# Performance work log

Measured on AMD Instinct MI355X. Metric: run time of the kernel, lower is better.

Reference implementation:

```python
import jax, jax.numpy as jnp
import numpy as np

U = 256    # hp.hidden_size * 2 (attention num_units / encoder dim)
H = 128    # hp.hidden_size (prenet output, attn GRU input)
MEL = 80   # hp.decoder_output_dim == hp.num_mels
R = 5      # hp.outputs_per_step
B = 64
T = 1000


def _glorot(key, shape):
    fan_in = shape[-1]
    return jax.random.normal(key, shape, jnp.float32) / jnp.sqrt(jnp.float32(fan_in))


def setup_inputs() -> dict:
    key = jax.random.key(0)
    ks = jax.random.split(key, 16)
    p = {}
    p["memory"] = jax.random.normal(ks[0], (B, T, U), jnp.float32)
    # prenet: fc1 (MEL->U), fc2 (U->H)
    p["Wp1"] = _glorot(ks[1], (U, MEL)); p["bp1"] = jnp.zeros((U,), jnp.float32)
    p["Wp2"] = _glorot(ks[2], (H, U));   p["bp2"] = jnp.zeros((H,), jnp.float32)
    # Bahdanau attention params (no bias)
    p["W1"] = _glorot(ks[3], (U, U))
    p["W2"] = _glorot(ks[4], (U, U))
    p["v"]  = _glorot(ks[5], (U,))
    def gru(k, din):
        k1, k2 = jax.random.split(k)
        return (_glorot(k1, (3 * U, din)), _glorot(k2, (3 * U, U)),
                jnp.zeros((3 * U,), jnp.float32), jnp.zeros((3 * U,), jnp.float32))
    p["Wa_ih"], p["Wa_hh"], p["ba_ih"], p["ba_hh"] = gru(ks[6], H)
    p["W1_ih"], p["W1_hh"], p["b1_ih"], p["b1_hh"] = gru(ks[7], U)
    p["W2_ih"], p["W2_hh"], p["b2_ih"], p["b2_hh"] = gru(ks[8], U)
    p["Wproj"] = _glorot(ks[9], (U, 2 * U)); p["bproj"] = jnp.zeros((U,), jnp.float32)
    p["Wout"] = _glorot(ks[10], (MEL * R, U)); p["bout"] = jnp.zeros((MEL * R,), jnp.float32)
    return p


def _gru_cell(x, h, W_ih, W_hh, b_ih, b_hh):
    # torch.nn.GRUCell semantics
    gi = x @ W_ih.T + b_ih
    gh = h @ W_hh.T + b_hh
    ir, iz, inn = jnp.split(gi, 3, axis=-1)
    hr, hz, hn = jnp.split(gh, 3, axis=-1)
    r = jax.nn.sigmoid(ir + hr)
    z = jax.nn.sigmoid(iz + hz)
    n = jnp.tanh(inn + r * hn)
    return (1.0 - z) * n + z * h


def reference(memory, Wp1, bp1, Wp2, bp2, W1, W2, v,
              Wa_ih, Wa_hh, ba_ih, ba_hh,
              W1_ih, W1_hh, b1_ih, b1_hh,
              W2_ih, W2_hh, b2_ih, b2_hh,
              Wproj, bproj, Wout, bout):
    b, t, u = memory.shape
    steps = t // R  # training branch: timesteps = memory_len // outputs_per_step
    # keys = W1(memory): constant across timesteps, hoist out of the loop
    keys = jnp.einsum('btu,vu->btv', memory, W1)
    init = (jnp.zeros((b, MEL), memory.dtype),  # prev mel frame (GO frame = zeros)
            jnp.zeros((b, u), memory.dtype),    # attn_hidden
            jnp.zeros((b, u), memory.dtype),    # gru1_hidden
            jnp.zeros((b, u), memory.dtype))    # gru2_hidden

    def step(carry, _):
        prev, attn_h, g1_h, g2_h = carry
        # prenet (dropout omitted for determinism; identity in eval mode)
        x = jax.nn.relu(prev @ Wp1.T + bp1)
        x = jax.nn.relu(x @ Wp2.T + bp2)
        # attention query through GRU cell
        d_t = _gru_cell(x, attn_h, Wa_ih, Wa_hh, ba_ih, ba_hh)
        q = d_t @ W2.T                                     # [b,u]
        scores = jnp.tanh(keys + q[:, None, :]) @ v       # [b,t]
        aw = jax.nn.softmax(scores, axis=1)
        d_t_prime = jnp.einsum('bt,btu->bu', aw, memory)   # context
        # residual GRU stack
        g1_in = jnp.concatenate([d_t, d_t_prime], axis=1) @ Wproj.T + bproj
        g1_h = _gru_cell(g1_in, g1_h, W1_ih, W1_hh, b1_ih, b1_hh)
        g2_in = g1_in + g1_h
        g2_h = _gru_cell(g2_in, g2_h, W2_ih, W2_hh, b2_ih, b2_hh)
        out = ((g2_in + g2_h) @ Wout.T + bout).reshape(b, MEL, R)
        return (out[:, :, -1], d_t, g1_h, g2_h), out

    _, ys = jax.lax.scan(step, init, None, length=steps)   # [steps,b,MEL,R]
    # torch.cat(outputs, 2) -> [b, MEL, steps*R]
    return jnp.transpose(ys, (1, 2, 0, 3)).reshape(b, MEL, steps * R)
```

## Files before the change

kernel.cpp:

```cpp
#include <hip/hip_runtime.h>

typedef _Float16 f16;
typedef _Float16 h2 __attribute__((ext_vector_type(2)));
typedef float fv4 __attribute__((ext_vector_type(4)));

#define BB 64
#define UU 256
#define RRR 5
#define NQUAD 4

constexpr size_t O_WP1T = 0;
constexpr size_t O_WP2T = 10240;
constexpr size_t O_WAIH = 26624;
constexpr size_t O_WAHH = 75776;
constexpr size_t O_WQP  = 174080;
constexpr size_t O_WPC  = 239616;
constexpr size_t O_W1IH = 272384;
constexpr size_t O_W1HH = 370688;
constexpr size_t O_W2IH = 468992;
constexpr size_t O_W2HH = 567296;
constexpr size_t O_WOUT = 665600;
constexpr size_t OF_BQP = 716800;
constexpr size_t OF_W1T = 717312;
constexpr size_t OH_KEYS = 1565696;
constexpr size_t OH_MEM  = OH_KEYS + 16384000;
constexpr size_t OF_CTXP  = 17166848;
constexpr size_t OF_ESUM  = 17297920;
constexpr size_t OI_FLAGS = 17298432;

#define SCL2LOG2E 2.8853900817779268f

#if defined(__has_builtin)
#if __has_builtin(__builtin_amdgcn_fdot2)
#define USE_FDOT2 1
#endif
#endif

__device__ __forceinline__ float dot2f(h2 a, h2 b, float c){
#ifdef USE_FDOT2
  return __builtin_amdgcn_fdot2(a, b, c, false);
#else
  return c + (float)a[0]*(float)b[0] + (float)a[1]*(float)b[1];
#endif
}

__device__ __forceinline__ float frcp(float x){ return __builtin_amdgcn_rcpf(x); }
__device__ __forceinline__ float fexp2(float x){ return __builtin_amdgcn_exp2f(x); }
__device__ __forceinline__ float fsig(float x){ return frcp(1.0f + fexp2(-1.4426950408889634f*x)); }
__device__ __forceinline__ float ftanh(float x){ return 1.0f - 2.0f*frcp(1.0f + fexp2(SCL2LOG2E*x)); }

__global__ void k_tr_hx(const float* __restrict__ src, int srcK, int kbase,
                        h2* __restrict__ dst, int N, int K, int Ntot, int coloff,
                        float scale){
  int idx = blockIdx.x*blockDim.x + threadIdx.x;
  int tot = N*(K/2);
  if (idx < tot){
    int k2 = idx / N, n = idx - k2*N;
    h2 p; p[0]=(f16)(scale*src[n*srcK + kbase + 2*k2]);
    p[1]=(f16)(scale*src[n*srcK + kbase + 2*k2+1]);
    dst[(size_t)k2*Ntot + coloff + n] = p;
  }
}

__global__ void k_transpose(const float* __restrict__ src, float* __restrict__ dst, int N, int K){
  int idx = blockIdx.x*blockDim.x + threadIdx.x;
  if (idx < N*K){
    int n = idx / K, k = idx - n*K;
    dst[k*N + n] = src[idx];
  }
}

__global__ void k_biasqp(const float* __restrict__ bproj, float* __restrict__ dst){
  int i = blockIdx.x*blockDim.x + threadIdx.x;
  if (i < 512) dst[i] = (i < 256) ? 0.f : bproj[i-256];
}

__global__ void k_zero(int* __restrict__ p, int n){
  int i = blockIdx.x*blockDim.x + threadIdx.x;
  if (i < n) p[i] = 0;
}

__global__ void k_memh(const float* __restrict__ src, f16* __restrict__ dst, int n8){
  int i = blockIdx.x*blockDim.x + threadIdx.x;
  if (i < n8){
    const float4* s = reinterpret_cast<const float4*>(src) + 2*(size_t)i;
    float4 f0 = s[0], f1 = s[1];
    union { f16 h[8]; float4 v; } u;
    u.h[0]=(f16)f0.x; u.h[1]=(f16)f0.y; u.h[2]=(f16)f0.z; u.h[3]=(f16)f0.w;
    u.h[4]=(f16)f1.x; u.h[5]=(f16)f1.y; u.h[6]=(f16)f1.z; u.h[7]=(f16)f1.w;
    reinterpret_cast<float4*>(dst)[i] = u.v;
  }
}

__global__ __launch_bounds__(256) void k_keys(const float* __restrict__ mem,
      const float* __restrict__ W1t, f16* __restrict__ keys, int T)
{
  const int b = blockIdx.z;
  const int tbase = blockIdx.x * 128;
  const int cbase = blockIdx.y * 128;
  const int tid = threadIdx.x;
  const int rt = tid >> 4, ct = tid & 15;
  const float* memb = mem + (size_t)b*T*UU;

  float acc[8][8];
  #pragma unroll
  for (int i=0;i<8;i++){
    #pragma unroll
    for (int j=0;j<8;j++) acc[i][j]=0.f;
  }
  const float* arow[8];
  #pragma unroll
  for (int i=0;i<8;i++){
    int t = tbase + rt*8 + i;
    arow[i] = memb + (size_t)(t < T ? t : T-1)*UU;
  }
  const float* wcol = W1t + cbase + ct*8;

  for (int k=0;k<UU;k+=4){
    float w8[4][8];
    #pragma unroll
    for (int kk=0;kk<4;kk++){
      float4 lo = *reinterpret_cast<const float4*>(wcol + (size_t)(k+kk)*UU);
      float4 hi = *reinterpret_cast<const float4*>(wcol + (size_t)(k+kk)*UU + 4);
      w8[kk][0]=lo.x; w8[kk][1]=lo.y; w8[kk][2]=lo.z; w8[kk][3]=lo.w;
      w8[kk][4]=hi.x; w8[kk][5]=hi.y; w8[kk][6]=hi.z; w8[kk][7]=hi.w;
    }
    #pragma unroll
    for (int i=0;i<8;i++){
      float4 a = *reinterpret_cast<const float4*>(arow[i] + k);
      float a4[4] = {a.x, a.y, a.z, a.w};
      #pragma unroll
      for (int kk=0;kk<4;kk++){
        #pragma unroll
        for (int j=0;j<8;j++) acc[i][j] += a4[kk]*w8[kk][j];
      }
    }
  }
  #pragma unroll
  for (int i=0;i<8;i++){
    int t = tbase + rt*8 + i;
    if (t < T){
      f16* dst = keys + (size_t)b*T*UU + (size_t)t*UU + cbase + ct*8;
      union { f16 h[8]; float4 v; } u;
      #pragma unroll
      for (int j=0;j<8;j++) u.h[j] = (f16)(acc[i][j]*SCL2LOG2E);
      *reinterpret_cast<float4*>(dst) = u.v;
    }
  }
}

__device__ __attribute__((noinline)) void gemv_shfl(
    const h2* __restrict__ W, const h2* __restrict__ in,
    const float* __restrict__ bias, float* __restrict__ destf, h2* __restrict__ desth,
    int K2, int Nf4, int act, int local)
{
  const int lane = local & 63;
  const int half = lane >> 5;
  int col = (local >> 6)*32 + (lane & 31);
  const bool valid = col < Nf4;
  if (!valid) col = 0;
  const int kh = K2 >> 1;
  const float4* w = reinterpret_cast<const float4*>(W) + (size_t)(half*kh)*Nf4 + col;
  const h2* ia = in + half*kh;
  float a0=0.f, a1=0.f, a2=0.f, a3=0.f;
  #pragma unroll 8
  for (int it = 0; it < kh; ++it){
    float4 wp = w[(size_t)it*Nf4];
    h2 a = ia[it];
    const h2* wh = reinterpret_cast<const h2*>(&wp);
    a0 = dot2f(wh[0], a, a0);
    a1 = dot2f(wh[1], a, a1);
    a2 = dot2f(wh[2], a, a2);
    a3 = dot2f(wh[3], a, a3);
  }
  a0 += __shfl_xor(a0, 32, 64);
  a1 += __shfl_xor(a1, 32, 64);
  a2 += __shfl_xor(a2, 32, 64);
  a3 += __shfl_xor(a3, 32, 64);
  if (half == 0 && valid){
    if (bias){
      const float4 bv = reinterpret_cast<const float4*>(bias)[col];
      a0+=bv.x; a1+=bv.y; a2+=bv.z; a3+=bv.w;
    }
    if (act == 1){
      a0=fmaxf(a0,0.f); a1=fmaxf(a1,0.f); a2=fmaxf(a2,0.f); a3=fmaxf(a3,0.f);
    } else if (act == 2){
      const float4 d = reinterpret_cast<float4*>(destf)[col];
      a0+=d.x; a1+=d.y; a2+=d.z; a3+=d.w;
    }
    if (destf){
      float4 r; r.x=a0; r.y=a1; r.z=a2; r.w=a3;
      reinterpret_cast<float4*>(destf)[col] = r;
    }
    if (desth){
      h2 p0; p0[0]=(f16)a0; p0[1]=(f16)a1;
      h2 p1; p1[0]=(f16)a2; p1[1]=(f16)a3;
      desth[2*col] = p0; desth[2*col+1] = p1;
    }
  }
}

__device__ __attribute__((noinline)) void gru_gate(
    const float* __restrict__ gi, const float* __restrict__ gh,
    float* __restrict__ h, h2* __restrict__ hh2,
    const float* __restrict__ addsrc, float* __restrict__ sumf,
    h2* __restrict__ sumh, int tid)
{
  if (tid < 128){
    float hn[2], sm[2] = {0.f, 0.f};
    #pragma unroll
    for (int d=0; d<2; ++d){
      int e = 2*tid + d;
      float r = fsig(gi[e] + gh[e]);
      float z = fsig(gi[256+e] + gh[256+e]);
      float n = ftanh(gi[512+e] + r*gh[512+e]);
      hn[d] = (1.f - z)*n + z*h[e];
      h[e] = hn[d];
      if (addsrc){ sm[d] = addsrc[e] + hn[d]; if (sumf) sumf[e] = sm[d]; }
    }
    h2 p; p[0]=(f16)hn[0]; p[1]=(f16)hn[1];
    hh2[tid] = p;
    if (addsrc && sumh){ h2 q; q[0]=(f16)sm[0]; q[1]=(f16)sm[1]; sumh[tid] = q; }
  }
  __syncthreads();
}

__global__ __launch_bounds__(1024) void k_decode(
    const h2* __restrict__ wts, const float* __restrict__ wsf,
    const f16* __restrict__ keysg, const f16* __restrict__ memg,
    float* __restrict__ ctxp, float* __restrict__ esum, int* __restrict__ flags,
    const float* __restrict__ bp1, const float* __restrict__ bp2,
    const float* __restrict__ vvec,
    const float* __restrict__ ba_ih, const float* __restrict__ ba_hh,
    const float* __restrict__ b1_ih, const float* __restrict__ b1_hh,
    const float* __restrict__ b2_ih, const float* __restrict__ b2_hh,
    const float* __restrict__ bout,
    float* __restrict__ out, int T, int steps)
{
  __shared__ __align__(16) float s_red[4096];
  __shared__ __align__(16) float s_sc[1024];
  __shared__ __align__(16) float s_gi[768];
  __shared__ __align__(16) float s_gh[768];
  __shared__ __align__(16) float s_gh1[768];
  __shared__ __align__(16) float s_gh2[768];
  __shared__ __align__(16) float s_q[512];
  __shared__ __align__(16) float s_ha[256];
  __shared__ __align__(16) float s_g1h[256];
  __shared__ __align__(16) float s_g2h[256];
  __shared__ __align__(16) float s_g2in[256];
  __shared__ __align__(16) float s_y[400];
  __shared__ __align__(16) f16   s_prevf[80];
  __shared__ __align__(16) h2    s_hah[128], s_g1hh[128], s_g2hh[128];
  __shared__ __align__(16) h2    s_g1inh[128], s_g2inh[128], s_s2h[128];
  __shared__ __align__(16) h2    s_x1h[128], s_xh[64], s_ctxh[128];
  __shared__ float s_wred[16];

  const int b    = blockIdx.x & 63;
  const int quad = blockIdx.x >> 6;
  const int tid = threadIdx.x;
  const int lane = tid & 63;
  const int wid = tid >> 6;
  const int half_id = lane >> 5;
  const int cl = lane & 31;

  const f16* keyb = keysg + (size_t)b*T*UU;
  const f16* memb = memg  + (size_t)b*T*UU;
  float* outb = out + (size_t)b*80*(steps*RRR);
  const int tq0 = (T*quad)/NQUAD, tq1 = (T*(quad+1))/NQUAD;

  if (tid < 128){
    s_ha[2*tid]=0.f; s_ha[2*tid+1]=0.f;
    s_g1h[2*tid]=0.f; s_g1h[2*tid+1]=0.f;
    s_g2h[2*tid]=0.f; s_g2h[2*tid+1]=0.f;
    h2 z; z[0]=(f16)0.f; z[1]=(f16)0.f;
    s_hah[tid]=z; s_g1hh[tid]=z; s_g2hh[tid]=z;
  }
  if (tid < 80) s_prevf[tid] = (f16)0.f;
  __syncthreads();

  float v8[8], m8[8];
  #pragma unroll
  for (int j=0;j<8;j++){ v8[j] = vvec[cl*8+j]; m8[j] = -2.0f*v8[j]; }
  float sumv = 0.f;
  #pragma unroll
  for (int j=0;j<8;j++) sumv += v8[j];
  #pragma unroll
  for (int o=1;o<32;o<<=1) sumv += __shfl_xor(sumv, o);

  for (int step = 0; step < steps; ++step){
    const int par = step & 1;
    if (tid < 384)      gemv_shfl(wts+O_WAHH, s_hah,  ba_hh, s_gh,  nullptr, 128, 192, 0, tid);
    else if (tid < 768) gemv_shfl(wts+O_W1HH, s_g1hh, b1_hh, s_gh1, nullptr, 128, 192, 0, tid-384);
    else if (tid < 896) gemv_shfl(wts+O_WP1T, reinterpret_cast<const h2*>(s_prevf), bp1,
                                  nullptr, s_x1h, 40, 64, 1, tid-768);
    __syncthreads();
    if (tid < 384)      gemv_shfl(wts+O_W2HH, s_g2hh, b2_hh, s_gh2, nullptr, 128, 192, 0, tid);
    else if (tid < 448) gemv_shfl(wts+O_WP2T, s_x1h, bp2, nullptr, s_xh, 128, 32, 1, tid-384);
    __syncthreads();
    if (tid < 384) gemv_shfl(wts+O_WAIH, s_xh, ba_ih, s_gi, nullptr, 64, 192, 0, tid);
    __syncthreads();
    gru_gate(s_gi, s_gh, s_ha, s_hah, nullptr, nullptr, nullptr, tid);
    if (tid < 256) gemv_shfl(wts+O_WQP, s_hah, wsf+OF_BQP, s_q, nullptr, 128, 128, 0, tid);
    __syncthreads();

    {
      float q8[8];
      #pragma unroll
      for (int j=0;j<8;j++) q8[j] = s_q[cl*8+j];
      float rs = 0.f;
      for (int t0 = tq0 + wid*2; t0 < tq1; t0 += 32){
        int t = t0 + half_id;
        fv4 kv = *(reinterpret_cast<const fv4*>(keyb + (size_t)t*UU) + cl);
        const h2* kh = reinterpret_cast<const h2*>(&kv);
        float acc = 0.f;
        #pragma unroll
        for (int p=0;p<4;p++){
          float t0f = (float)kh[p][0] + q8[2*p];
          float t1f = (float)kh[p][1] + q8[2*p+1];
          acc = fmaf(m8[2*p],   frcp(1.f + fexp2(t0f)), acc);
          acc = fmaf(m8[2*p+1], frcp(1.f + fexp2(t1f)), acc);
        }
        #pragma unroll
        for (int o=1;o<32;o<<=1) acc += __shfl_xor(acc, o);
        float e = __expf(sumv + acc);
        if (cl == 0) s_sc[t] = e;
        rs += e;
      }
      rs += __shfl_xor(rs, 32);
      if (lane==0) s_wred[wid] = rs;
    }
    __syncthreads();
    {
      float c8[8] = {0.f,0.f,0.f,0.f,0.f,0.f,0.f,0.f};
      for (int t0 = tq0 + wid*2; t0 < tq1; t0 += 32){
        int t = t0 + half_id;
        float wgt = s_sc[t];
        fv4 mv = *(reinterpret_cast<const fv4*>(memb + (size_t)t*UU) + cl);
        const h2* mh = reinterpret_cast<const h2*>(&mv);
        #pragma unroll
        for (int p=0;p<4;p++){
          c8[2*p  ] += wgt*(float)mh[p][0];
          c8[2*p+1] += wgt*(float)mh[p][1];
        }
      }
      #pragma unroll
      for (int j=0;j<8;j++) c8[j] += __shfl_xor(c8[j], 32);
      if (half_id == 0){
        float4 lo; lo.x=c8[0]; lo.y=c8[1]; lo.z=c8[2]; lo.w=c8[3];
        float4 hi; hi.x=c8[4]; hi.y=c8[5]; hi.z=c8[6]; hi.w=c8[7];
        *reinterpret_cast<float4*>(s_red + wid*256 + cl*8)     = lo;
        *reinterpret_cast<float4*>(s_red + wid*256 + cl*8 + 4) = hi;
      }
    }
    __syncthreads();
    {
      float* cp = ctxp + (((size_t)b*2 + par)*NQUAD + quad)*256;
      if (tid < 128){
        float a = 0.f, c = 0.f;
        #pragma unroll
        for (int w=0; w<16; ++w){
          a += s_red[w*256 + 2*tid];
          c += s_red[w*256 + 2*tid+1];
        }
        cp[2*tid]   = a;
        cp[2*tid+1] = c;
      }
      if (tid == 0){
        float tot = 0.f;
        #pragma unroll
        for (int w=0; w<16; ++w) tot += s_wred[w];
        esum[((size_t)b*2 + par)*NQUAD + quad] = tot;
      }
    }
    __syncthreads();
    if (tid == 0){
      int* fl = flags + b*256 + step;
      __threadfence();
      __hip_atomic_fetch_add(fl, 1, __ATOMIC_RELEASE, __HIP_MEMORY_SCOPE_AGENT);
      while (__hip_atomic_load(fl, __ATOMIC_ACQUIRE, __HIP_MEMORY_SCOPE_AGENT) < NQUAD){
        __builtin_amdgcn_s_sleep(2);
      }
    }
    __syncthreads();
    if (tid < 128){
      const float* cp0 = ctxp + ((size_t)b*2 + par)*NQUAD*256;
      const float* es0 = esum + ((size_t)b*2 + par)*NQUAD;
      float es = 0.f;
      #pragma unroll
      for (int q4=0;q4<NQUAD;q4++)
        es += __hip_atomic_load(&es0[q4], __ATOMIC_RELAXED, __HIP_MEMORY_SCOPE_AGENT);
      float inv = frcp(es);
      float a = 0.f, c = 0.f;
      #pragma unroll
      for (int q4=0;q4<NQUAD;q4++){
        a += __hip_atomic_load(&cp0[q4*256 + 2*tid],   __ATOMIC_RELAXED, __HIP_MEMORY_SCOPE_AGENT);
        c += __hip_atomic_load(&cp0[q4*256 + 2*tid+1], __ATOMIC_RELAXED, __HIP_MEMORY_SCOPE_AGENT);
      }
      h2 p; p[0]=(f16)(a*inv); p[1]=(f16)(c*inv);
      s_ctxh[tid] = p;
    }
    __syncthreads();

    if (tid < 128) gemv_shfl(wts+O_WPC, s_ctxh, nullptr, s_q+256, s_g1inh, 128, 64, 2, tid);
    __syncthreads();
    if (tid < 384) gemv_shfl(wts+O_W1IH, s_g1inh, b1_ih, s_gi, nullptr, 128, 192, 0, tid);
    __syncthreads();
    gru_gate(s_gi, s_gh1, s_g1h, s_g1hh, s_q+256, s_g2in, s_g2inh, tid);
    if (tid < 384) gemv_shfl(wts+O_W2IH, s_g2inh, b2_ih, s_gi, nullptr, 128, 192, 0, tid);
    __syncthreads();
    gru_gate(s_gi, s_gh2, s_g2h, s_g2hh, s_g2in, nullptr, s_s2h, tid);
    if (tid < 256) gemv_shfl(wts+O_WOUT, s_s2h, bout, s_y, nullptr, 128, 100, 0, tid);
    __syncthreads();
    if (tid < 400){
      float val = s_y[tid];
      int mel = tid / 5, rr = tid - mel*5;
      if (quad == 0)
        __builtin_nontemporal_store(val, &outb[(size_t)mel*(steps*RRR) + step*RRR + rr]);
      if (rr == 4) s_prevf[mel] = (f16)val;
    }
    __syncthreads();
  }
}

extern "C" void kernel_launch(void* const* d_in, const int* in_sizes, int n_in,
                              void* d_out, int out_size, void* d_ws, size_t ws_size,
                              hipStream_t stream)
{
  const float* mem  = (const float*)d_in[0];
  const float* Wp1  = (const float*)d_in[1];
  const float* bp1  = (const float*)d_in[2];
  const float* Wp2  = (const float*)d_in[3];
  const float* bp2  = (const float*)d_in[4];
  const float* W1   = (const float*)d_in[5];
  const float* W2   = (const float*)d_in[6];
  const float* vv   = (const float*)d_in[7];
  const float* Wa_ih= (const float*)d_in[8];
  const float* Wa_hh= (const float*)d_in[9];
  const float* ba_ih= (const float*)d_in[10];
  const float* ba_hh= (const float*)d_in[11];
  const float* W1_ih= (const float*)d_in[12];
  const float* W1_hh= (const float*)d_in[13];
  const float* b1_ih= (const float*)d_in[14];
  const float* b1_hh= (const float*)d_in[15];
  const float* W2_ih= (const float*)d_in[16];
  const float* W2_hh= (const float*)d_in[17];
  const float* b2_ih= (const float*)d_in[18];
  const float* b2_hh= (const float*)d_in[19];
  const float* Wproj= (const float*)d_in[20];
  const float* bproj= (const float*)d_in[21];
  const float* Wout = (const float*)d_in[22];
  const float* bout = (const float*)d_in[23];

  h2*  wsH2 = (h2*)d_ws;
  f16* wsF16= (f16*)d_ws;
  float* wsF = (float*)d_ws;
  int*  wsI = (int*)d_ws;
  int T = in_sizes[0] / (BB*UU);
  int steps = T / RRR;

  auto tr = [&](const float* src, int srcK, int kbase, size_t off, int N, int K,
                int Ntot, int coloff, float scale){
    int total = N*(K/2);
    k_tr_hx<<<dim3((total+255)/256), dim3(256), 0, stream>>>(
        src, srcK, kbase, wsH2 + off, N, K, Ntot, coloff, scale);
  };
  tr(Wp1,   80,  0, O_WP1T, 256, 80,  256, 0, 1.f);
  tr(Wp2,   256, 0, O_WP2T, 128, 256, 128, 0, 1.f);
  tr(Wa_ih, 128, 0, O_WAIH, 768, 128, 768, 0, 1.f);
  tr(Wa_hh, 256, 0, O_WAHH, 768, 256, 768, 0, 1.f);
  tr(W2,    256, 0, O_WQP,  256, 256, 512, 0, SCL2LOG2E);
  tr(Wproj, 512, 0, O_WQP,  256, 256, 512, 256, 1.f);
  tr(Wproj, 512, 256, O_WPC, 256, 256, 256, 0, 1.f);
  tr(W1_ih, 256, 0, O_W1IH, 768, 256, 768, 0, 1.f);
  tr(W1_hh, 256, 0, O_W1HH, 768, 256, 768, 0, 1.f);
  tr(W2_ih, 256, 0, O_W2IH, 768, 256, 768, 0, 1.f);
  tr(W2_hh, 256, 0, O_W2HH, 768, 256, 768, 0, 1.f);
  tr(Wout,  256, 0, O_WOUT, 400, 256, 400, 0, 1.f);

  k_biasqp<<<dim3(2), dim3(256), 0, stream>>>(bproj, wsF + OF_BQP);
  k_transpose<<<dim3((256*256+255)/256), dim3(256), 0, stream>>>(W1, wsF + OF_W1T, 256, 256);
  k_zero<<<dim3(64), dim3(256), 0, stream>>>(wsI + OI_FLAGS, 64*256);

  int n8 = (BB*T*UU)/8;
  k_memh<<<dim3((n8+255)/256), dim3(256), 0, stream>>>(mem, wsF16 + OH_MEM, n8);
  k_keys<<<dim3((T+127)/128, UU/128, BB), dim3(256), 0, stream>>>(mem, wsF + OF_W1T, wsF16 + OH_KEYS, T);

  k_decode<<<dim3(BB*NQUAD), dim3(1024), 0, stream>>>(wsH2, wsF,
      wsF16 + OH_KEYS, wsF16 + OH_MEM,
      wsF + OF_CTXP, wsF + OF_ESUM, wsI + OI_FLAGS,
      bp1, bp2, vv, ba_ih, ba_hh, b1_ih, b1_hh, b2_ih, b2_hh, bout,
      (float*)d_out, T, steps);
}
```

Baseline: 12.43 ms.

## Make quad 0 the sole recurrent leader and broadcast queries to attention workers

Before, all four blocks per batch row ran the whole recurrent GRU chain redundantly. Now only block quad 0 runs it. It publishes the attention query through a global buffer and flag A, and the other three blocks only wait, compute their attention slice and signal flag B. The small GEMVs also move to a new 4-way K-split variant that uses more threads and shuffle reductions. This shortens the serial per-step chain, at the cost of an extra cross-block handoff each step.

```diff
diff --git a/kernel.cpp b/kernel.cpp
--- a/kernel.cpp
+++ b/kernel.cpp
@@ -26,7 +26,9 @@
 constexpr size_t OH_MEM  = OH_KEYS + 16384000;
 constexpr size_t OF_CTXP  = 17166848;
 constexpr size_t OF_ESUM  = 17297920;
-constexpr size_t OI_FLAGS = 17298432;
+constexpr size_t OF_QB    = 17298432;
+constexpr size_t OI_FLAGA = 17331200;
+constexpr size_t OI_FLAGB = 17347584;
 
 #define SCL2LOG2E 2.8853900817779268f
 
@@ -200,6 +202,57 @@
   }
 }
 
+__device__ __attribute__((noinline)) void gemv_shfl4(
+    const h2* __restrict__ W, const h2* __restrict__ in,
+    const float* __restrict__ bias, float* __restrict__ destf, h2* __restrict__ desth,
+    int K2, int Nf4, int act, int local)
+{
+  const int lane = local & 63;
+  const int qtr  = lane >> 4;
+  int col = (local >> 6)*16 + (lane & 15);
+  const bool valid = col < Nf4;
+  if (!valid) col = 0;
+  const int kq = K2 >> 2;
+  const float4* w = reinterpret_cast<const float4*>(W) + (size_t)(qtr*kq)*Nf4 + col;
+  const h2* ia = in + qtr*kq;
+  float a0=0.f, a1=0.f, a2=0.f, a3=0.f;
+  #pragma unroll 8
+  for (int it = 0; it < kq; ++it){
+    float4 wp = w[(size_t)it*Nf4];
+    h2 a = ia[it];
+    const h2* wh = reinterpret_cast<const h2*>(&wp);
+    a0 = dot2f(wh[0], a, a0);
+    a1 = dot2f(wh[1], a, a1);
+    a2 = dot2f(wh[2], a, a2);
+    a3 = dot2f(wh[3], a, a3);
+  }
+  a0 += __shfl_xor(a0, 16, 64); a1 += __shfl_xor(a1, 16, 64);
+  a2 += __shfl_xor(a2, 16, 64); a3 += __shfl_xor(a3, 16, 64);
+  a0 += __shfl_xor(a0, 32, 64); a1 += __shfl_xor(a1, 32, 64);
+  a2 += __shfl_xor(a2, 32, 64); a3 += __shfl_xor(a3, 32, 64);
+  if (qtr == 0 && valid){
+    if (bias){
+      const float4 bv = reinterpret_cast<const float4*>(bias)[col];
+      a0+=bv.x; a1+=bv.y; a2+=bv.z; a3+=bv.w;
+    }
+    if (act == 1){
+      a0=fmaxf(a0,0.f); a1=fmaxf(a1,0.f); a2=fmaxf(a2,0.f); a3=fmaxf(a3,0.f);
+    } else if (act == 2){
+      const float4 d = reinterpret_cast<float4*>(destf)[col];
+      a0+=d.x; a1+=d.y; a2+=d.z; a3+=d.w;
+    }
+    if (destf){
+      float4 r; r.x=a0; r.y=a1; r.z=a2; r.w=a3;
+      reinterpret_cast<float4*>(destf)[col] = r;
+    }
+    if (desth){
+      h2 p0; p0[0]=(f16)a0; p0[1]=(f16)a1;
+      h2 p1; p1[0]=(f16)a2; p1[1]=(f16)a3;
+      desth[2*col] = p0; desth[2*col+1] = p1;
+    }
+  }
+}
+
 __device__ __attribute__((noinline)) void gru_gate(
     const float* __restrict__ gi, const float* __restrict__ gh,
     float* __restrict__ h, h2* __restrict__ hh2,
@@ -228,7 +281,8 @@
 __global__ __launch_bounds__(1024) void k_decode(
     const h2* __restrict__ wts, const float* __restrict__ wsf,
     const f16* __restrict__ keysg, const f16* __restrict__ memg,
-    float* __restrict__ ctxp, float* __restrict__ esum, int* __restrict__ flags,
+    float* __restrict__ ctxp, float* __restrict__ esum, float* __restrict__ qbuf,
+    int* __restrict__ flagA, int* __restrict__ flagB,
     const float* __restrict__ bp1, const float* __restrict__ bp2,
     const float* __restrict__ vvec,
     const float* __restrict__ ba_ih, const float* __restrict__ ba_hh,
@@ -268,16 +322,6 @@
   float* outb = out + (size_t)b*80*(steps*RRR);
   const int tq0 = (T*quad)/NQUAD, tq1 = (T*(quad+1))/NQUAD;
 
-  if (tid < 128){
-    s_ha[2*tid]=0.f; s_ha[2*tid+1]=0.f;
-    s_g1h[2*tid]=0.f; s_g1h[2*tid+1]=0.f;
-    s_g2h[2*tid]=0.f; s_g2h[2*tid+1]=0.f;
-    h2 z; z[0]=(f16)0.f; z[1]=(f16)0.f;
-    s_hah[tid]=z; s_g1hh[tid]=z; s_g2hh[tid]=z;
-  }
-  if (tid < 80) s_prevf[tid] = (f16)0.f;
-  __syncthreads();
-
   float v8[8], m8[8];
   #pragma unroll
   for (int j=0;j<8;j++){ v8[j] = vvec[cl*8+j]; m8[j] = -2.0f*v8[j]; }
@@ -287,22 +331,7 @@
   #pragma unroll
   for (int o=1;o<32;o<<=1) sumv += __shfl_xor(sumv, o);
 
-  for (int step = 0; step < steps; ++step){
-    const int par = step & 1;
-    if (tid < 384)      gemv_shfl(wts+O_WAHH, s_hah,  ba_hh, s_gh,  nullptr, 128, 192, 0, tid);
-    else if (tid < 768) gemv_shfl(wts+O_W1HH, s_g1hh, b1_hh, s_gh1, nullptr, 128, 192, 0, tid-384);
-    else if (tid < 896) gemv_shfl(wts+O_WP1T, reinterpret_cast<const h2*>(s_prevf), bp1,
-                                  nullptr, s_x1h, 40, 64, 1, tid-768);
-    __syncthreads();
-    if (tid < 384)      gemv_shfl(wts+O_W2HH, s_g2hh, b2_hh, s_gh2, nullptr, 128, 192, 0, tid);
-    else if (tid < 448) gemv_shfl(wts+O_WP2T, s_x1h, bp2, nullptr, s_xh, 128, 32, 1, tid-384);
-    __syncthreads();
-    if (tid < 384) gemv_shfl(wts+O_WAIH, s_xh, ba_ih, s_gi, nullptr, 64, 192, 0, tid);
-    __syncthreads();
-    gru_gate(s_gi, s_gh, s_ha, s_hah, nullptr, nullptr, nullptr, tid);
-    if (tid < 256) gemv_shfl(wts+O_WQP, s_hah, wsf+OF_BQP, s_q, nullptr, 128, 128, 0, tid);
-    __syncthreads();
-
+  auto attn_slice = [&](int par){
     {
       float q8[8];
       #pragma unroll
@@ -373,11 +402,70 @@
       }
     }
     __syncthreads();
+  };
+
+  if (quad != 0){
+    for (int step = 0; step < steps; ++step){
+      const int par = step & 1;
+      if (tid == 0){
+        const int* fa = flagA + b*256 + step;
+        while (__hip_atomic_load(fa, __ATOMIC_ACQUIRE, __HIP_MEMORY_SCOPE_AGENT) < 1){
+          __builtin_amdgcn_s_sleep(2);
+        }
+      }
+      __syncthreads();
+      if (tid < 256)
+        s_q[tid] = __hip_atomic_load(qbuf + ((size_t)b*2 + par)*256 + tid,
+                                     __ATOMIC_RELAXED, __HIP_MEMORY_SCOPE_AGENT);
+      __syncthreads();
+      attn_slice(par);
+      if (tid == 0){
+        __threadfence();
+        __hip_atomic_fetch_add(flagB + b*256 + step, 1, __ATOMIC_RELEASE, __HIP_MEMORY_SCOPE_AGENT);
+      }
+      __syncthreads();
+    }
+    return;
+  }
+
+  if (tid < 128){
+    s_ha[2*tid]=0.f; s_ha[2*tid+1]=0.f;
+    s_g1h[2*tid]=0.f; s_g1h[2*tid+1]=0.f;
+    s_g2h[2*tid]=0.f; s_g2h[2*tid+1]=0.f;
+    h2 z; z[0]=(f16)0.f; z[1]=(f16)0.f;
+    s_hah[tid]=z; s_g1hh[tid]=z; s_g2hh[tid]=z;
+  }
+  if (tid < 80) s_prevf[tid] = (f16)0.f;
+  __syncthreads();
+
+  for (int step = 0; step < steps; ++step){
+    const int par = step & 1;
+    if (tid < 384)      gemv_shfl (wts+O_WAHH, s_hah,  ba_hh, s_gh,  nullptr, 128, 192, 0, tid);
+    else if (tid < 768) gemv_shfl (wts+O_W1HH, s_g1hh, b1_hh, s_gh1, nullptr, 128, 192, 0, tid-384);
+    else                gemv_shfl4(wts+O_WP1T, reinterpret_cast<const h2*>(s_prevf), bp1,
+                                   nullptr, s_x1h, 40, 64, 1, tid-768);
+    __syncthreads();
+    if (tid < 768)      gemv_shfl4(wts+O_W2HH, s_g2hh, b2_hh, s_gh2, nullptr, 128, 192, 0, tid);
+    else if (tid < 896) gemv_shfl4(wts+O_WP2T, s_x1h, bp2, nullptr, s_xh, 128, 32, 1, tid-768);
+    __syncthreads();
+    if (tid < 768) gemv_shfl4(wts+O_WAIH, s_xh, ba_ih, s_gi, nullptr, 64, 192, 0, tid);
+    __syncthreads();
+    gru_gate(s_gi, s_gh, s_ha, s_hah, nullptr, nullptr, nullptr, tid);
+    if (tid < 512) gemv_shfl4(wts+O_WQP, s_hah, wsf+OF_BQP, s_q, nullptr, 128, 128, 0, tid);
+    __syncthreads();
+    if (tid < 256)
+      qbuf[((size_t)b*2 + par)*256 + tid] = s_q[tid];
+    __syncthreads();
     if (tid == 0){
-      int* fl = flags + b*256 + step;
       __threadfence();
-      __hip_atomic_fetch_add(fl, 1, __ATOMIC_RELEASE, __HIP_MEMORY_SCOPE_AGENT);
-      while (__hip_atomic_load(fl, __ATOMIC_ACQUIRE, __HIP_MEMORY_SCOPE_AGENT) < NQUAD){
+      __hip_atomic_fetch_add(flagA + b*256 + step, 1, __ATOMIC_RELEASE, __HIP_MEMORY_SCOPE_AGENT);
+    }
+    attn_slice(par);
+    if (tid == 0){
+      __threadfence();
+      __hip_atomic_fetch_add(flagB + b*256 + step, 1, __ATOMIC_RELEASE, __HIP_MEMORY_SCOPE_AGENT);
+      const int* fb = flagB + b*256 + step;
+      while (__hip_atomic_load(fb, __ATOMIC_ACQUIRE, __HIP_MEMORY_SCOPE_AGENT) < NQUAD){
         __builtin_amdgcn_s_sleep(2);
       }
     }
@@ -400,22 +488,20 @@
       s_ctxh[tid] = p;
     }
     __syncthreads();
-
-    if (tid < 128) gemv_shfl(wts+O_WPC, s_ctxh, nullptr, s_q+256, s_g1inh, 128, 64, 2, tid);
-    __syncthreads();
-    if (tid < 384) gemv_shfl(wts+O_W1IH, s_g1inh, b1_ih, s_gi, nullptr, 128, 192, 0, tid);
+    if (tid < 256) gemv_shfl4(wts+O_WPC, s_ctxh, nullptr, s_q+256, s_g1inh, 128, 64, 2, tid);
+    __syncthreads();
+    if (tid < 768) gemv_shfl4(wts+O_W1IH, s_g1inh, b1_ih, s_gi, nullptr, 128, 192, 0, tid);
     __syncthreads();
     gru_gate(s_gi, s_gh1, s_g1h, s_g1hh, s_q+256, s_g2in, s_g2inh, tid);
-    if (tid < 384) gemv_shfl(wts+O_W2IH, s_g2inh, b2_ih, s_gi, nullptr, 128, 192, 0, tid);
+    if (tid < 768) gemv_shfl4(wts+O_W2IH, s_g2inh, b2_ih, s_gi, nullptr, 128, 192, 0, tid);
     __syncthreads();
     gru_gate(s_gi, s_gh2, s_g2h, s_g2hh, s_g2in, nullptr, s_s2h, tid);
-    if (tid < 256) gemv_shfl(wts+O_WOUT, s_s2h, bout, s_y, nullptr, 128, 100, 0, tid);
+    if (tid < 448) gemv_shfl4(wts+O_WOUT, s_s2h, bout, s_y, nullptr, 128, 100, 0, tid);
     __syncthreads();
     if (tid < 400){
       float val = s_y[tid];
       int mel = tid / 5, rr = tid - mel*5;
-      if (quad == 0)
-        __builtin_nontemporal_store(val, &outb[(size_t)mel*(steps*RRR) + step*RRR + rr]);
+      __builtin_nontemporal_store(val, &outb[(size_t)mel*(steps*RRR) + step*RRR + rr]);
       if (rr == 4) s_prevf[mel] = (f16)val;
     }
     __syncthreads();
@@ -479,7 +565,7 @@
 
   k_biasqp<<<dim3(2), dim3(256), 0, stream>>>(bproj, wsF + OF_BQP);
   k_transpose<<<dim3((256*256+255)/256), dim3(256), 0, stream>>>(W1, wsF + OF_W1T, 256, 256);
-  k_zero<<<dim3(64), dim3(256), 0, stream>>>(wsI + OI_FLAGS, 64*256);
+  k_zero<<<dim3(128), dim3(256), 0, stream>>>(wsI + OI_FLAGA, 2*64*256);
 
   int n8 = (BB*T*UU)/8;
   k_memh<<<dim3((n8+255)/256), dim3(256), 0, stream>>>(mem, wsF16 + OH_MEM, n8);
@@ -487,7 +573,8 @@
 
   k_decode<<<dim3(BB*NQUAD), dim3(1024), 0, stream>>>(wsH2, wsF,
       wsF16 + OH_KEYS, wsF16 + OH_MEM,
-      wsF + OF_CTXP, wsF + OF_ESUM, wsI + OI_FLAGS,
+      wsF + OF_CTXP, wsF + OF_ESUM, wsF + OF_QB,
+      wsI + OI_FLAGA, wsI + OI_FLAGB,
       bp1, bp2, vv, ba_ih, ba_hh, b1_ih, b1_hh, b2_ih, b2_hh, bout,
       (float*)d_out, T, steps);
 }
```

Result: slower. 49.52 ms (+298.5%).
